# Kernel tuning notes

Hardware: AMD Instinct MI355X
Metric: run time of the kernel (lower is better)

## Reference

```python
import jax, jax.numpy as jnp
import numpy as np


def setup_inputs() -> dict:
    key = jax.random.key(0)
    x = jax.random.normal(key, (4, 3, 8192), dtype=jnp.float32)  # (B, 3, N)
    return {"x": x, "k": 30}


def reference(x, k):
    # x: (B, 3, N)
    x_t = jnp.swapaxes(x, 1, 2)  # (B, N, 3)
    xx = jnp.sum(x_t ** 2, axis=2, keepdims=True)  # (B, N, 1)
    # pairwise squared distances (B, N, N)
    pairwise = xx + jnp.swapaxes(xx, 1, 2) - 2.0 * jnp.matmul(x_t, x)
    # k smallest distances -> negate and take top_k
    _, idx = jax.lax.top_k(-pairwise, k)  # idx: (B, N, k)
    # gather neighbors: (B, N, k, 3)
    neighbors = jax.vmap(lambda pts, i: pts[i])(x_t, idx)
    centroid = jnp.mean(neighbors, axis=2, keepdims=True)  # (B, N, 1, 3)
    centered = neighbors - centroid  # (B, N, k, 3)
    # per-point 3x3 covariance
    cov = jnp.einsum('bnki,bnkj->bnij', centered, centered)  # (B, N, 3, 3)
    _, v = jnp.linalg.eigh(cov)  # eigenvalues ascending
    normals = v[..., :, 0]  # eigenvector of smallest eigenvalue, (B, N, 3)
    # orient normals toward viewpoint (origin): view_dir = -x_t
    dot = jnp.sum(-x_t * normals, axis=-1, keepdims=True)
    normals = jnp.where(dot < 0, -normals, normals)
    x_out = jnp.concatenate([x, jnp.swapaxes(normals, 1, 2)], axis=1)  # (B, 6, N)
    return x_out
```

## Files before the change

### kernel.cpp

```cpp
#include <hip/hip_runtime.h>
#include <math.h>

#define N_PTS   8192
#define KNN     30
#define CAPG    104
#define STR     105
#define GROUPS  8
#define BLOCK   128
#define NZ      64
#define NY      64
#define NBKT    (NZ * NY)
#define CLO     -4.0f
#define CSC     8.0f
#define LAMBDA  48.0f


__device__ __forceinline__ int clampi(int v, int lo, int hi) {
    return v < lo ? lo : (v > hi ? hi : v);
}
__device__ __forceinline__ int bucket_of(float pz, float py) {
    int zb = clampi((int)floorf((pz - CLO) * CSC), 0, NZ - 1);
    int yb = clampi((int)floorf((py - CLO) * CSC), 0, NY - 1);
    return (zb << 6) | yb;
}

__global__ __launch_bounds__(1024) void prep_kernel(const float* __restrict__ x,
                                                    float4* __restrict__ S,
                                                    int* __restrict__ O,
                                                    int* __restrict__ bstart,
                                                    float* __restrict__ out) {
    __shared__ int hist[NBKT];
    __shared__ int cur[NBKT];
    __shared__ int wsum[16];

    const int b = blockIdx.x;
    const int t = threadIdx.x;
    const int wid = t >> 6, lane = t & 63;
    const float* xb = x + (size_t)b * 3 * N_PTS;
    float* ob = out + (size_t)b * 6 * N_PTS;

    for (int k = t; k < NBKT; k += 1024) hist[k] = 0;
    __syncthreads();

    float px[8], py[8], pz[8];
    int   bk[8];
    #pragma unroll
    for (int u = 0; u < 8; ++u) {
        int i = (u << 10) + t;
        px[u] = xb[i]; py[u] = xb[N_PTS + i]; pz[u] = xb[2 * N_PTS + i];
        bk[u] = bucket_of(pz[u], py[u]);
        atomicAdd(&hist[bk[u]], 1);
        ob[i]             = px[u];
        ob[N_PTS + i]     = py[u];
        ob[2 * N_PTS + i] = pz[u];
    }
    __syncthreads();

    int l0 = hist[4 * t], l1 = hist[4 * t + 1], l2 = hist[4 * t + 2], l3 = hist[4 * t + 3];
    int s = l0 + l1 + l2 + l3;
    int sum = s;
    #pragma unroll
    for (int off = 1; off < 64; off <<= 1) {
        int v = __shfl_up(sum, off);
        if (lane >= off) sum += v;
    }
    if (lane == 63) wsum[wid] = sum;
    __syncthreads();
    if (t == 0) {
        int run = 0;
        #pragma unroll
        for (int k = 0; k < 16; ++k) { int v = wsum[k]; wsum[k] = run; run += v; }
    }
    __syncthreads();
    int base = wsum[wid] + (sum - s);
    int b0 = base, b1 = base + l0, b2 = b1 + l1, b3 = b2 + l2;
    cur[4 * t] = b0; cur[4 * t + 1] = b1; cur[4 * t + 2] = b2; cur[4 * t + 3] = b3;
    int* bsb = bstart + b * (NBKT + 1);
    bsb[4 * t] = b0; bsb[4 * t + 1] = b1; bsb[4 * t + 2] = b2; bsb[4 * t + 3] = b3;
    if (t == 1023) bsb[NBKT] = N_PTS;
    __syncthreads();

    float4* Sb = S + ((size_t)b << 13);
    int*    Ob = O + ((size_t)b << 13);
    #pragma unroll
    for (int u = 0; u < 8; ++u) {
        int dst = atomicAdd(&cur[bk[u]], 1);
        float xx = __fadd_rn(__fadd_rn(__fmul_rn(px[u], px[u]), __fmul_rn(py[u], py[u])),
                             __fmul_rn(pz[u], pz[u]));
        Sb[dst] = make_float4(px[u], py[u], pz[u], xx);
        Ob[dst] = (u << 10) + t;
    }
}

__global__ __launch_bounds__(BLOCK, 6) void knn_normal_kernel(const float4* __restrict__ S,
                                                              const int* __restrict__ O,
                                                              const int* __restrict__ bstart,
                                                              float* __restrict__ out) {
    __shared__ unsigned long long ldk[GROUPS * STR];

    const int t    = threadIdx.x;
    const int l16  = t & 15;
    const int g    = t >> 4;
    const int gsh  = (t & 63) & ~15;
    const int qblk = (blockIdx.x * 1031) & 4095;
    const int qid  = qblk * GROUPS + g;
    const int b    = qid >> 13;
    const int pos  = qid & (N_PTS - 1);
    const float4* __restrict__ P  = S + ((size_t)b << 13);
    const int*    __restrict__ Ob = O + ((size_t)b << 13);
    const int*    __restrict__ bs = bstart + b * (NBKT + 1);
    const float4 qp = P[pos];
    const int    oi = Ob[pos];

    unsigned long long* __restrict__ ldg = ldk + g * STR;

    const float c = fmaxf(sqrtf(qp.w), 1e-3f);
    float rlo = 0.05f, rhi = 6.0f;
    for (int it = 0; it < 14; ++it) {
        float r = 0.5f * (rlo + rhi);
        float slo = fmaxf(c - r, 0.0f);
        float h = (c + r - slo) * 0.125f;
        float f = 0.0f;
        if (l16 <= 8) {
            float sq = slo + h * (float)l16;
            float cs = c - sq;
            float hh = fmaxf(fminf((r * r - cs * cs) * (0.5f / c), 2.0f * sq), 0.0f);
            float w = (l16 == 0 || l16 == 8) ? 1.0f : ((l16 & 1) ? 4.0f : 2.0f);
            f = w * __expf(-0.5f * sq * sq) * sq * hh;
        }
        f += __shfl_xor(f, 1, 16); f += __shfl_xor(f, 2, 16);
        f += __shfl_xor(f, 4, 16); f += __shfl_xor(f, 8, 16);
        float lam = 1089.3f * f * h;
        if (lam < LAMBDA) rlo = r; else rhi = r;
    }
    float rad = rhi * 1.02f;
    float r2  = rad * rad;

    int  cnt = 0;
    bool active = true;

    for (;;) {
        if (active) {
            cnt = 0;
            float w = __fmaf_rn(sqrtf(r2), 1.002f, 1e-3f);
            int zlo = clampi((int)floorf((qp.z - w - CLO) * CSC), 0, NZ - 1);
            int zhi = clampi((int)floorf((qp.z + w - CLO) * CSC), 0, NZ - 1);
            int ylo = clampi((int)floorf((qp.y - w - CLO) * CSC), 0, NY - 1);
            int yhi = clampi((int)floorf((qp.y + w - CLO) * CSC), 0, NY - 1);
            for (int zb = zlo; zb <= zhi; ++zb) {
                int lo = bs[(zb << 6) + ylo];
                int hi = bs[(zb << 6) + yhi + 1];
                int smax = (hi - lo + 31) >> 5;
                for (int s = 0; s < smax; ++s) {
                    int j1  = lo + (s << 5) + l16;
                    int j2  = j1 + 16;
                    int jc1 = j1 < hi ? j1 : hi - 1;
                    int jc2 = j2 < hi ? j2 : hi - 1;
                    float4 p1 = P[jc1];
                    float4 p2 = P[jc2];
                    float mm1 = __fmaf_rn(qp.z, p1.z, __fmaf_rn(qp.y, p1.y, __fmul_rn(qp.x, p1.x)));
                    float d1  = __fsub_rn(__fadd_rn(qp.w, p1.w), __fmul_rn(2.0f, mm1));
                    float mm2 = __fmaf_rn(qp.z, p2.z, __fmaf_rn(qp.y, p2.y, __fmul_rn(qp.x, p2.x)));
                    float d2  = __fsub_rn(__fadd_rn(qp.w, p2.w), __fmul_rn(2.0f, mm2));
                    bool hit1 = (j1 < hi) && (d1 <= r2);
                    bool hit2 = (j2 < hi) && (d2 <= r2);
                    unsigned long long m1 = __ballot(hit1);
                    unsigned sub1 = (unsigned)((m1 >> gsh) & 0xFFFFull);
                    if (hit1) {
                        int slot = cnt + __popc(sub1 & ((1u << l16) - 1u));
                        if (slot < CAPG) {
                            unsigned u = __float_as_uint(d1);
                            u = (u & 0x80000000u) ? ~u : (u | 0x80000000u);
                            ldg[slot] = ((unsigned long long)u << 28) | (unsigned long long)jc1;
                        }
                    }
                    cnt += __popc(sub1);
                    unsigned long long m2 = __ballot(hit2);
                    unsigned sub2 = (unsigned)((m2 >> gsh) & 0xFFFFull);
                    if (hit2) {
                        int slot = cnt + __popc(sub2 & ((1u << l16) - 1u));
                        if (slot < CAPG) {
                            unsigned u = __float_as_uint(d2);
                            u = (u & 0x80000000u) ? ~u : (u | 0x80000000u);
                            ldg[slot] = ((unsigned long long)u << 28) | (unsigned long long)jc2;
                        }
                    }
                    cnt += __popc(sub2);
                }
            }
        }
        bool bad = active && (cnt < KNN || cnt > CAPG);
        if (__ballot(bad) == 0ULL) break;
        active = bad;
        if (active) r2 = (cnt < KNN) ? r2 * 1.6f : r2 * 0.82f;
    }

    for (int k = l16; k < cnt; k += 16) {
        unsigned long long key = ldg[k];
        int jc = (int)(key & 0x3FFFull);
        ldg[k] = (key & ~0x0FFFFFFFull) | ((unsigned long long)Ob[jc] << 14) | (unsigned long long)jc;
    }
    __syncthreads();

    const double qx = (double)qp.x, qy = (double)qp.y, qz = (double)qp.z;
    double sx = 0.0, sy = 0.0, sz = 0.0;
    double sxx = 0.0, sxy = 0.0, sxz = 0.0, syy = 0.0, syz = 0.0, szz = 0.0;

    for (int k = l16; k < cnt; k += 16) {
        unsigned long long key = ldg[k];
        int rank = 0;
        for (int u = 0; u < cnt; ++u) rank += (ldg[u] < key) ? 1 : 0;
        if (rank < KNN) {
            float4 p = P[(int)(key & 0x3FFFull)];
            double ax = (double)p.x - qx, ay = (double)p.y - qy, az = (double)p.z - qz;
            sx += ax; sy += ay; sz += az;
            sxx = fma(ax, ax, sxx); sxy = fma(ax, ay, sxy); sxz = fma(ax, az, sxz);
            syy = fma(ay, ay, syy); syz = fma(ay, az, syz); szz = fma(az, az, szz);
        }
    }

    #pragma unroll
    for (int off = 1; off < 16; off <<= 1) {
        sx  += __shfl_xor(sx,  off, 16); sy  += __shfl_xor(sy,  off, 16); sz  += __shfl_xor(sz,  off, 16);
        sxx += __shfl_xor(sxx, off, 16); sxy += __shfl_xor(sxy, off, 16); sxz += __shfl_xor(sxz, off, 16);
        syy += __shfl_xor(syy, off, 16); syz += __shfl_xor(syz, off, 16); szz += __shfl_xor(szz, off, 16);
    }

    if (l16 == 0) {
        const double kinv = 1.0 / (double)KNN;
        double m00 = sxx - sx * sx * kinv;
        double m11 = syy - sy * sy * kinv;
        double m22 = szz - sz * sz * kinv;
        double m01 = sxy - sx * sy * kinv;
        double m02 = sxz - sx * sz * kinv;
        double m12 = syz - sy * sz * kinv;

        double nx = 1.0, ny = 0.0, nz = 0.0;
        double q3 = (m00 + m11 + m22) / 3.0;
        double p1 = m01 * m01 + m02 * m02 + m12 * m12;
        double d00 = m00 - q3, d11 = m11 - q3, d22 = m22 - q3;
        double p2 = d00 * d00 + d11 * d11 + d22 * d22 + 2.0 * p1;
        if (p2 > 1e-280) {
            double pp = sqrt(p2 / 6.0);
            double ip = 1.0 / pp;
            double b00 = d00 * ip, b11 = d11 * ip, b22 = d22 * ip;
            double b01 = m01 * ip, b02 = m02 * ip, b12 = m12 * ip;
            double detB = b00 * (b11 * b22 - b12 * b12)
                        - b01 * (b01 * b22 - b12 * b02)
                        + b02 * (b01 * b12 - b11 * b02);
            double rr = 0.5 * detB;
            rr = rr < -1.0 ? -1.0 : (rr > 1.0 ? 1.0 : rr);
            double phi = acos(rr) / 3.0;
            double lam = q3 + 2.0 * pp * cos(phi + 2.0943951023931953);
            double a00 = m00 - lam, a11 = m11 - lam, a22 = m22 - lam;
            double v0x = m01 * m12 - m02 * a11, v0y = m02 * m01 - a00 * m12, v0z = a00 * a11 - m01 * m01;
            double v1x = m01 * a22 - m02 * m12, v1y = m02 * m02 - a00 * a22, v1z = a00 * m12 - m01 * m02;
            double v2x = a11 * a22 - m12 * m12, v2y = m12 * m02 - m01 * a22, v2z = m01 * m12 - a11 * m02;
            double n0 = v0x * v0x + v0y * v0y + v0z * v0z;
            double n1 = v1x * v1x + v1y * v1y + v1z * v1z;
            double n2 = v2x * v2x + v2y * v2y + v2z * v2z;
            double bx = v0x, by = v0y, bz = v0z, bn = n0;
            if (n1 > bn) { bx = v1x; by = v1y; bz = v1z; bn = n1; }
            if (n2 > bn) { bx = v2x; by = v2y; bz = v2z; bn = n2; }
            if (bn > 1e-280) {
                double inv = 1.0 / sqrt(bn);
                nx = bx * inv; ny = by * inv; nz = bz * inv;
            }
        }
        double dq = -(qx * nx + qy * ny + qz * nz);
        if (dq < 0.0) { nx = -nx; ny = -ny; nz = -nz; }

        float* ob = out + (size_t)b * 6 * N_PTS;
        ob[3 * N_PTS + oi] = (float)nx;
        ob[4 * N_PTS + oi] = (float)ny;
        ob[5 * N_PTS + oi] = (float)nz;
    }
}

extern "C" void kernel_launch(void* const* d_in, const int* in_sizes, int n_in,
                              void* d_out, int out_size, void* d_ws, size_t ws_size,
                              hipStream_t stream) {
    const float* x = (const float*)d_in[0];
    float* out = (float*)d_out;
    char* ws = (char*)d_ws;
    float4* S    = (float4*)(ws);
    int*    O    = (int*)(ws + 524288);
    int*    bsta = (int*)(ws + 655360);

    prep_kernel<<<dim3(4), dim3(1024), 0, stream>>>(x, S, O, bsta, out);
    knn_normal_kernel<<<dim3(32768 / GROUPS), dim3(BLOCK), 0, stream>>>(S, O, bsta, out);
}
```

Before: 164.5 us.

## Split bucket-sort prep into parallel histogram, scan and scatter kernels

The single 4-block prep kernel that built the spatial bucket sort is replaced by three kernels: a 128-block global-atomic histogram (which also copies xyz to the output), a small per-batch scan, and a 128-block scatter. This spreads the serial per-batch prep across many CUs instead of four. The cost is extra launches, a memset, global atomics and rereading x. The KNN query-to-block mapping also changes from a scrambled permutation to a strided one, so each block now handles queries from different batches, which changes load balance and cache locality.

```diff
diff --git a/kernel.cpp b/kernel.cpp
--- a/kernel.cpp
+++ b/kernel.cpp
@@ -24,72 +24,66 @@
     return (zb << 6) | yb;
 }
 
-__global__ __launch_bounds__(1024) void prep_kernel(const float* __restrict__ x,
-                                                    float4* __restrict__ S,
-                                                    int* __restrict__ O,
-                                                    int* __restrict__ bstart,
-                                                    float* __restrict__ out) {
-    __shared__ int hist[NBKT];
-    __shared__ int cur[NBKT];
-    __shared__ int wsum[16];
-
-    const int b = blockIdx.x;
-    const int t = threadIdx.x;
-    const int wid = t >> 6, lane = t & 63;
+__global__ __launch_bounds__(256) void hist_kernel(const float* __restrict__ x,
+                                                   int* __restrict__ hist,
+                                                   float* __restrict__ out) {
+    int gid = blockIdx.x * 256 + threadIdx.x;
+    int b = gid >> 13, i = gid & (N_PTS - 1);
     const float* xb = x + (size_t)b * 3 * N_PTS;
+    float px = xb[i], py = xb[N_PTS + i], pz = xb[2 * N_PTS + i];
     float* ob = out + (size_t)b * 6 * N_PTS;
-
-    for (int k = t; k < NBKT; k += 1024) hist[k] = 0;
-    __syncthreads();
-
-    float px[8], py[8], pz[8];
-    int   bk[8];
-    #pragma unroll
-    for (int u = 0; u < 8; ++u) {
-        int i = (u << 10) + t;
-        px[u] = xb[i]; py[u] = xb[N_PTS + i]; pz[u] = xb[2 * N_PTS + i];
-        bk[u] = bucket_of(pz[u], py[u]);
-        atomicAdd(&hist[bk[u]], 1);
-        ob[i]             = px[u];
-        ob[N_PTS + i]     = py[u];
-        ob[2 * N_PTS + i] = pz[u];
-    }
-    __syncthreads();
-
-    int l0 = hist[4 * t], l1 = hist[4 * t + 1], l2 = hist[4 * t + 2], l3 = hist[4 * t + 3];
-    int s = l0 + l1 + l2 + l3;
+    ob[i]             = px;
+    ob[N_PTS + i]     = py;
+    ob[2 * N_PTS + i] = pz;
+    atomicAdd(&hist[b * NBKT + bucket_of(pz, py)], 1);
+}
+
+__global__ __launch_bounds__(256) void scan_kernel(const int* __restrict__ hist,
+                                                   int* __restrict__ bstart,
+                                                   int* __restrict__ cur) {
+    __shared__ int wtot[4];
+    const int b = blockIdx.x, t = threadIdx.x;
+    const int lane = t & 63, wid = t >> 6;
+    const int* h = hist + b * NBKT;
+    int base = t * 16;
+    int s = 0;
+    #pragma unroll
+    for (int k = 0; k < 16; ++k) s += h[base + k];
     int sum = s;
     #pragma unroll
     for (int off = 1; off < 64; off <<= 1) {
         int v = __shfl_up(sum, off);
         if (lane >= off) sum += v;
     }
-    if (lane == 63) wsum[wid] = sum;
+    if (lane == 63) wtot[wid] = sum;
     __syncthreads();
-    if (t == 0) {
-        int run = 0;
-        #pragma unroll
-        for (int k = 0; k < 16; ++k) { int v = wsum[k]; wsum[k] = run; run += v; }
-    }
-    __syncthreads();
-    int base = wsum[wid] + (sum - s);
-    int b0 = base, b1 = base + l0, b2 = b1 + l1, b3 = b2 + l2;
-    cur[4 * t] = b0; cur[4 * t + 1] = b1; cur[4 * t + 2] = b2; cur[4 * t + 3] = b3;
+    int wbase = 0;
+    #pragma unroll
+    for (int k = 0; k < 4; ++k) wbase += (k < wid) ? wtot[k] : 0;
+    int run = wbase + sum - s;
     int* bsb = bstart + b * (NBKT + 1);
-    bsb[4 * t] = b0; bsb[4 * t + 1] = b1; bsb[4 * t + 2] = b2; bsb[4 * t + 3] = b3;
-    if (t == 1023) bsb[NBKT] = N_PTS;
-    __syncthreads();
-
-    float4* Sb = S + ((size_t)b << 13);
-    int*    Ob = O + ((size_t)b << 13);
-    #pragma unroll
-    for (int u = 0; u < 8; ++u) {
-        int dst = atomicAdd(&cur[bk[u]], 1);
-        float xx = __fadd_rn(__fadd_rn(__fmul_rn(px[u], px[u]), __fmul_rn(py[u], py[u])),
-                             __fmul_rn(pz[u], pz[u]));
-        Sb[dst] = make_float4(px[u], py[u], pz[u], xx);
-        Ob[dst] = (u << 10) + t;
-    }
+    #pragma unroll
+    for (int k = 0; k < 16; ++k) {
+        bsb[base + k] = run;
+        cur[b * NBKT + base + k] = run;
+        run += h[base + k];
+    }
+    if (t == 255) bsb[NBKT] = N_PTS;
+}
+
+__global__ __launch_bounds__(256) void scatter_kernel(const float* __restrict__ x,
+                                                      float4* __restrict__ S,
+                                                      int* __restrict__ O,
+                                                      int* __restrict__ cur) {
+    int gid = blockIdx.x * 256 + threadIdx.x;
+    int b = gid >> 13, i = gid & (N_PTS - 1);
+    const float* xb = x + (size_t)b * 3 * N_PTS;
+    float px = xb[i], py = xb[N_PTS + i], pz = xb[2 * N_PTS + i];
+    float xx = __fadd_rn(__fadd_rn(__fmul_rn(px, px), __fmul_rn(py, py)),
+                         __fmul_rn(pz, pz));
+    int dst = atomicAdd(&cur[b * NBKT + bucket_of(pz, py)], 1);
+    S[(b << 13) + dst] = make_float4(px, py, pz, xx);
+    O[(b << 13) + dst] = i;
 }
 
 __global__ __launch_bounds__(BLOCK, 6) void knn_normal_kernel(const float4* __restrict__ S,
@@ -102,8 +96,7 @@
     const int l16  = t & 15;
     const int g    = t >> 4;
     const int gsh  = (t & 63) & ~15;
-    const int qblk = (blockIdx.x * 1031) & 4095;
-    const int qid  = qblk * GROUPS + g;
+    const int qid  = blockIdx.x + (g << 12);
     const int b    = qid >> 13;
     const int pos  = qid & (N_PTS - 1);
     const float4* __restrict__ P  = S + ((size_t)b << 13);
@@ -286,7 +279,12 @@
     float4* S    = (float4*)(ws);
     int*    O    = (int*)(ws + 524288);
     int*    bsta = (int*)(ws + 655360);
-
-    prep_kernel<<<dim3(4), dim3(1024), 0, stream>>>(x, S, O, bsta, out);
-    knn_normal_kernel<<<dim3(32768 / GROUPS), dim3(BLOCK), 0, stream>>>(S, O, bsta, out);
-}
+    int*    hist = (int*)(ws + 720912);
+    int*    cur  = (int*)(ws + 786448);
+
+    hipMemsetAsync(hist, 0, 4 * NBKT * sizeof(int), stream);
+    hist_kernel<<<dim3(128), dim3(256), 0, stream>>>(x, hist, out);
+    scan_kernel<<<dim3(4), dim3(256), 0, stream>>>(hist, bsta, cur);
+    scatter_kernel<<<dim3(128), dim3(256), 0, stream>>>(x, S, O, cur);
+    knn_normal_kernel<<<dim3(4096), dim3(BLOCK), 0, stream>>>(S, O, bsta, out);
+}
```

New measurement: 174.4 us. 6.0% more time.
